# Kernel optimization log

Hardware: AMD Instinct MI355X
Metric: run time of the kernel (lower is better)

## Reference

```python
import jax, jax.numpy as jnp
import numpy as np

N = 4096       # number of nodes (generalizes the hardcoded 116)
E = 131072     # number of edges (avg degree 32)
F_IN = 128     # node_features_num
FS = 64        # feature_size
H = 8          # pair-MLP hidden width


def setup_inputs() -> dict:
    key = jax.random.key(0)
    ks = jax.random.split(key, 6)
    x = jax.random.normal(ks[0], (N, F_IN), dtype=jnp.float32)
    Wlin = jax.random.normal(ks[1], (FS, F_IN), dtype=jnp.float32) * 0.08
    blin = jnp.zeros((FS,), dtype=jnp.float32)
    W1 = jax.random.normal(ks[2], (H, 2 * FS), dtype=jnp.float32) * 0.08
    b1 = jnp.zeros((H,), dtype=jnp.float32)
    W2 = jax.random.normal(ks[3], (1, H), dtype=jnp.float32) * 0.3
    b2 = jnp.zeros((1,), dtype=jnp.float32)
    edge_index = jax.random.randint(ks[4], (2, E), 0, N, dtype=jnp.int32)
    # uniform noise for the concrete/Gumbel-sigmoid sample (torch.rand)
    u = jax.random.uniform(ks[5], (E,), dtype=jnp.float32, minval=1e-6, maxval=1.0 - 1e-6)
    return dict(x=x, Wlin=Wlin, blin=blin, W1=W1, b1=b1, W2=W2, b2=b2,
                edge_index=edge_index, u=u)


def reference(x, Wlin, blin, W1, b1, W2, b2, edge_index, u):
    # node embedding: Linear(F_IN, FS)
    x64 = x @ Wlin.T + blin                                # [N, FS]
    # all-pairs concat + Linear(2*FS, H) rewritten as two small matmuls
    # + broadcasted add (exactly equivalent math, avoids [N*N, 2*FS]).
    h1 = x64 @ W1[:, :FS].T                                # [N, H]
    h2 = x64 @ W1[:, FS:].T                                # [N, H]
    pair = jax.nn.sigmoid(h1[:, None, :] + h2[None, :, :] + b1)  # [N, N, H]
    score = jax.nn.sigmoid(jnp.einsum('ijh,h->ij', pair, W2[0]) + b2[0])  # [N, N]
    sym = 0.5 * (score + score.T)
    w = sym[edge_index[0], edge_index[1]]                  # [E]
    # _sample_graph, training=True, temperature=0.5, bias=0.0 -> bias=1e-4
    bias = 0.0001
    eps = (2.0 * bias - 1.0) * u + (1.0 - bias)            # eps in (1e-4, 1-1e-4)
    gate = jax.nn.sigmoid((jnp.log(eps) - jnp.log1p(-eps) + w) / 0.5)
    pos_penalty = jnp.var(gate, ddof=1)                    # torch.var is unbiased
    return gate, pos_penalty
```

## Files before the change

kernel.cpp:

```cpp
#include <hip/hip_runtime.h>
#include <math.h>

#define NNODES 4096
#define EEDGES 131072
#define FIN    128
#define FS     64

__device__ __forceinline__ float sigmoidf_(float x) {
    return 1.0f / (1.0f + __expf(-x));
}

__global__ void fuse_weights(const float* __restrict__ W1,
                             const float* __restrict__ Wlin,
                             const float* __restrict__ blin,
                             const float* __restrict__ b1,
                             float* __restrict__ M,
                             float* __restrict__ dvec) {
    int idx = blockIdx.x * blockDim.x + threadIdx.x;
    if (idx < 16 * FIN) {
        int k = idx >> 7;
        int c = idx & 127;
        const float* w1row = (k < 8) ? (W1 + k * 128) : (W1 + (k - 8) * 128 + 64);
        float acc = 0.f;
        #pragma unroll 8
        for (int f = 0; f < FS; ++f)
            acc = fmaf(w1row[f], Wlin[f * FIN + c], acc);
        M[idx] = acc;
    } else if (idx < 16 * FIN + 16) {
        int k = idx - 16 * FIN;
        const float* w1row = (k < 8) ? (W1 + k * 128) : (W1 + (k - 8) * 128 + 64);
        float acc = 0.f;
        #pragma unroll 8
        for (int f = 0; f < FS; ++f)
            acc = fmaf(w1row[f], blin[f], acc);
        if (k < 8) acc += b1[k];
        dvec[k] = acc;
    }
}

__global__ void node_mlp(const float* __restrict__ x,
                         const float* __restrict__ M,
                         const float* __restrict__ dvec,
                         float* __restrict__ h) {
    int t = blockIdx.x * blockDim.x + threadIdx.x;
    int n = t >> 4;
    int k = t & 15;
    const float4* xr = (const float4*)(x + n * FIN);
    const float4* mr = (const float4*)(M + k * FIN);
    float acc = dvec[k];
    #pragma unroll
    for (int q = 0; q < FIN / 4; ++q) {
        float4 a = xr[q];
        float4 b = mr[q];
        acc = fmaf(a.x, b.x, acc);
        acc = fmaf(a.y, b.y, acc);
        acc = fmaf(a.z, b.z, acc);
        acc = fmaf(a.w, b.w, acc);
    }
    h[t] = acc;
}

__global__ void edge_kernel(const float* __restrict__ h,
                            const int* __restrict__ ei,
                            const float* __restrict__ u,
                            const float* __restrict__ W2,
                            const float* __restrict__ b2,
                            float* __restrict__ gate,
                            float* __restrict__ partials) {
    int e = blockIdx.x * blockDim.x + threadIdx.x;
    int i = ei[e];
    int j = ei[EEDGES + e];

    const float4* hi = (const float4*)(h + i * 16);
    const float4* hj = (const float4*)(h + j * 16);
    float A1[8], A2[8], B1[8], B2[8];
    *(float4*)(A1)     = hi[0];  *(float4*)(A1 + 4) = hi[1];
    *(float4*)(A2)     = hi[2];  *(float4*)(A2 + 4) = hi[3];
    *(float4*)(B1)     = hj[0];  *(float4*)(B1 + 4) = hj[1];
    *(float4*)(B2)     = hj[2];  *(float4*)(B2 + 4) = hj[3];

    float w2v[8];
    *(float4*)(w2v)     = ((const float4*)W2)[0];
    *(float4*)(w2v + 4) = ((const float4*)W2)[1];
    float b2v = b2[0];

    float tij = 0.f, tji = 0.f;
    #pragma unroll
    for (int k = 0; k < 8; ++k) {
        tij = fmaf(w2v[k], sigmoidf_(A1[k] + B2[k]), tij);
        tji = fmaf(w2v[k], sigmoidf_(B1[k] + A2[k]), tji);
    }
    float sij = sigmoidf_(tij + b2v);
    float sji = sigmoidf_(tji + b2v);
    float w = 0.5f * (sij + sji);

    float uv = u[e];
    float eps = fmaf(-0.9998f, uv, 0.9999f);
    float logit = __logf(eps) - log1pf(-eps);
    float g = sigmoidf_(2.0f * (logit + w));
    gate[e] = g;

    float s = g, s2 = g * g;
    #pragma unroll
    for (int off = 32; off > 0; off >>= 1) {
        s  += __shfl_down(s,  off, 64);
        s2 += __shfl_down(s2, off, 64);
    }
    __shared__ float ls[4], ls2[4];
    int wave = threadIdx.x >> 6;
    if ((threadIdx.x & 63) == 0) { ls[wave] = s; ls2[wave] = s2; }
    __syncthreads();
    if (threadIdx.x == 0) {
        float ts = ls[0] + ls[1] + ls[2] + ls[3];
        float ts2 = ls2[0] + ls2[1] + ls2[2] + ls2[3];
        partials[blockIdx.x] = ts;
        partials[512 + blockIdx.x] = ts2;
    }
}

__global__ void finalize(const float* __restrict__ partials,
                         float* __restrict__ out) {
    int t = threadIdx.x;
    float s  = partials[t]       + partials[t + 256];
    float s2 = partials[512 + t] + partials[512 + t + 256];
    #pragma unroll
    for (int off = 32; off > 0; off >>= 1) {
        s  += __shfl_down(s,  off, 64);
        s2 += __shfl_down(s2, off, 64);
    }
    __shared__ float ls[4], ls2[4];
    int wave = t >> 6;
    if ((t & 63) == 0) { ls[wave] = s; ls2[wave] = s2; }
    __syncthreads();
    if (t == 0) {
        float S  = ls[0] + ls[1] + ls[2] + ls[3];
        float S2 = ls2[0] + ls2[1] + ls2[2] + ls2[3];
        const float Ef = (float)EEDGES;
        float var = (S2 - S * S / Ef) / (Ef - 1.0f);
        out[EEDGES] = var;
    }
}

extern "C" void kernel_launch(void* const* d_in, const int* in_sizes, int n_in,
                              void* d_out, int out_size, void* d_ws, size_t ws_size,
                              hipStream_t stream) {
    const float* x    = (const float*)d_in[0];
    const float* Wlin = (const float*)d_in[1];
    const float* blin = (const float*)d_in[2];
    const float* W1   = (const float*)d_in[3];
    const float* b1   = (const float*)d_in[4];
    const float* W2   = (const float*)d_in[5];
    const float* b2   = (const float*)d_in[6];
    const int*   ei   = (const int*)d_in[7];
    const float* u    = (const float*)d_in[8];
    float* out = (float*)d_out;

    float* ws       = (float*)d_ws;
    float* M        = ws;
    float* dvec     = ws + 2048;
    float* h        = ws + 2064;
    float* partials = ws + 2064 + 65536;

    fuse_weights<<<9, 256, 0, stream>>>(W1, Wlin, blin, b1, M, dvec);
    node_mlp<<<256, 256, 0, stream>>>(x, M, dvec, h);
    edge_kernel<<<512, 256, 0, stream>>>(h, ei, u, W2, b2, out, partials);
    finalize<<<1, 256, 0, stream>>>(partials, out);
}
```

Measured before the change: 87.85 us.

## Fuse weight folding into node kernel and finalize into edge kernel

Each node block now recomputes the folded weight matrix into shared memory instead of using a separate kernel, removing one launch. The variance finalize is folded into the edge kernel through a last-block-done atomic counter, removing another launch. log1pf is replaced by a direct log of a precomputed 1-eps. In exchange every node block does redundant weight folding (about 2K dot products of length 64), and the finalize now depends on correct fence and atomic ordering.

```diff
diff --git a/kernel.cpp b/kernel.cpp
--- a/kernel.cpp
+++ b/kernel.cpp
@@ -5,49 +5,56 @@
 #define EEDGES 131072
 #define FIN    128
 #define FS     64
+#define EBLOCKS 512
 
 __device__ __forceinline__ float sigmoidf_(float x) {
     return 1.0f / (1.0f + __expf(-x));
 }
 
-__global__ void fuse_weights(const float* __restrict__ W1,
-                             const float* __restrict__ Wlin,
-                             const float* __restrict__ blin,
-                             const float* __restrict__ b1,
-                             float* __restrict__ M,
-                             float* __restrict__ dvec) {
-    int idx = blockIdx.x * blockDim.x + threadIdx.x;
-    if (idx < 16 * FIN) {
-        int k = idx >> 7;
-        int c = idx & 127;
+__global__ __launch_bounds__(256) void fused_node(
+        const float* __restrict__ x,
+        const float* __restrict__ Wlin,
+        const float* __restrict__ blin,
+        const float* __restrict__ W1,
+        const float* __restrict__ b1,
+        float* __restrict__ h,
+        unsigned int* __restrict__ counter) {
+    __shared__ float Msh[16 * 132];
+    __shared__ float dsh[16];
+    int tid = threadIdx.x;
+
+    if (blockIdx.x == 0 && tid == 0) {
+        __hip_atomic_store(counter, 0u, __ATOMIC_RELAXED, __HIP_MEMORY_SCOPE_AGENT);
+    }
+
+    #pragma unroll
+    for (int p = 0; p < 8; ++p) {
+        int e = tid + p * 256;
+        int k = e >> 7;
+        int c = e & 127;
         const float* w1row = (k < 8) ? (W1 + k * 128) : (W1 + (k - 8) * 128 + 64);
         float acc = 0.f;
-        #pragma unroll 8
+        #pragma unroll 16
         for (int f = 0; f < FS; ++f)
             acc = fmaf(w1row[f], Wlin[f * FIN + c], acc);
-        M[idx] = acc;
-    } else if (idx < 16 * FIN + 16) {
-        int k = idx - 16 * FIN;
+        Msh[k * 132 + c] = acc;
+    }
+    if (tid < 16) {
+        int k = tid;
         const float* w1row = (k < 8) ? (W1 + k * 128) : (W1 + (k - 8) * 128 + 64);
-        float acc = 0.f;
-        #pragma unroll 8
+        float acc = (k < 8) ? b1[k] : 0.f;
+        #pragma unroll 16
         for (int f = 0; f < FS; ++f)
             acc = fmaf(w1row[f], blin[f], acc);
-        if (k < 8) acc += b1[k];
-        dvec[k] = acc;
+        dsh[k] = acc;
     }
-}
+    __syncthreads();
 
-__global__ void node_mlp(const float* __restrict__ x,
-                         const float* __restrict__ M,
-                         const float* __restrict__ dvec,
-                         float* __restrict__ h) {
-    int t = blockIdx.x * blockDim.x + threadIdx.x;
-    int n = t >> 4;
-    int k = t & 15;
+    int n = (blockIdx.x << 4) + (tid >> 4);
+    int k = tid & 15;
     const float4* xr = (const float4*)(x + n * FIN);
-    const float4* mr = (const float4*)(M + k * FIN);
-    float acc = dvec[k];
+    const float4* mr = (const float4*)(Msh + k * 132);
+    float acc = dsh[k];
     #pragma unroll
     for (int q = 0; q < FIN / 4; ++q) {
         float4 a = xr[q];
@@ -57,22 +64,25 @@
         acc = fmaf(a.z, b.z, acc);
         acc = fmaf(a.w, b.w, acc);
     }
-    h[t] = acc;
+    h[(n << 4) + k] = acc;
 }
 
-__global__ void edge_kernel(const float* __restrict__ h,
-                            const int* __restrict__ ei,
-                            const float* __restrict__ u,
-                            const float* __restrict__ W2,
-                            const float* __restrict__ b2,
-                            float* __restrict__ gate,
-                            float* __restrict__ partials) {
-    int e = blockIdx.x * blockDim.x + threadIdx.x;
+__global__ __launch_bounds__(256) void edge_kernel(
+        const float* __restrict__ h,
+        const int* __restrict__ ei,
+        const float* __restrict__ u,
+        const float* __restrict__ W2,
+        const float* __restrict__ b2,
+        float* __restrict__ out,
+        float* __restrict__ partials,
+        unsigned int* __restrict__ counter) {
+    int tid = threadIdx.x;
+    int e = blockIdx.x * 256 + tid;
     int i = ei[e];
     int j = ei[EEDGES + e];
 
-    const float4* hi = (const float4*)(h + i * 16);
-    const float4* hj = (const float4*)(h + j * 16);
+    const float4* hi = (const float4*)(h + (i << 4));
+    const float4* hj = (const float4*)(h + (j << 4));
     float A1[8], A2[8], B1[8], B2[8];
     *(float4*)(A1)     = hi[0];  *(float4*)(A1 + 4) = hi[1];
     *(float4*)(A2)     = hi[2];  *(float4*)(A2 + 4) = hi[3];
@@ -90,15 +100,14 @@
         tij = fmaf(w2v[k], sigmoidf_(A1[k] + B2[k]), tij);
         tji = fmaf(w2v[k], sigmoidf_(B1[k] + A2[k]), tji);
     }
-    float sij = sigmoidf_(tij + b2v);
-    float sji = sigmoidf_(tji + b2v);
-    float w = 0.5f * (sij + sji);
+    float w = 0.5f * (sigmoidf_(tij + b2v) + sigmoidf_(tji + b2v));
 
     float uv = u[e];
-    float eps = fmaf(-0.9998f, uv, 0.9999f);
-    float logit = __logf(eps) - log1pf(-eps);
+    float eps       = fmaf(-0.9998f, uv, 0.9999f);
+    float one_m_eps = fmaf( 0.9998f, uv, 0.0001f);
+    float logit = __logf(eps) - __logf(one_m_eps);
     float g = sigmoidf_(2.0f * (logit + w));
-    gate[e] = g;
+    out[e] = g;
 
     float s = g, s2 = g * g;
     #pragma unroll
@@ -107,37 +116,41 @@
         s2 += __shfl_down(s2, off, 64);
     }
     __shared__ float ls[4], ls2[4];
-    int wave = threadIdx.x >> 6;
-    if ((threadIdx.x & 63) == 0) { ls[wave] = s; ls2[wave] = s2; }
+    int wave = tid >> 6;
+    if ((tid & 63) == 0) { ls[wave] = s; ls2[wave] = s2; }
     __syncthreads();
-    if (threadIdx.x == 0) {
-        float ts = ls[0] + ls[1] + ls[2] + ls[3];
+
+    __shared__ unsigned int lastFlag;
+    if (tid == 0) {
+        float ts  = ls[0] + ls[1] + ls[2] + ls[3];
         float ts2 = ls2[0] + ls2[1] + ls2[2] + ls2[3];
-        partials[blockIdx.x] = ts;
-        partials[512 + blockIdx.x] = ts2;
+        __hip_atomic_store(&partials[blockIdx.x],       ts,  __ATOMIC_RELAXED, __HIP_MEMORY_SCOPE_AGENT);
+        __hip_atomic_store(&partials[EBLOCKS + blockIdx.x], ts2, __ATOMIC_RELAXED, __HIP_MEMORY_SCOPE_AGENT);
+        __threadfence();
+        unsigned int old = __hip_atomic_fetch_add(counter, 1u, __ATOMIC_ACQ_REL, __HIP_MEMORY_SCOPE_AGENT);
+        lastFlag = (old == (unsigned)(gridDim.x - 1)) ? 1u : 0u;
     }
-}
+    __syncthreads();
 
-__global__ void finalize(const float* __restrict__ partials,
-                         float* __restrict__ out) {
-    int t = threadIdx.x;
-    float s  = partials[t]       + partials[t + 256];
-    float s2 = partials[512 + t] + partials[512 + t + 256];
-    #pragma unroll
-    for (int off = 32; off > 0; off >>= 1) {
-        s  += __shfl_down(s,  off, 64);
-        s2 += __shfl_down(s2, off, 64);
-    }
-    __shared__ float ls[4], ls2[4];
-    int wave = t >> 6;
-    if ((t & 63) == 0) { ls[wave] = s; ls2[wave] = s2; }
-    __syncthreads();
-    if (t == 0) {
-        float S  = ls[0] + ls[1] + ls[2] + ls[3];
-        float S2 = ls2[0] + ls2[1] + ls2[2] + ls2[3];
-        const float Ef = (float)EEDGES;
-        float var = (S2 - S * S / Ef) / (Ef - 1.0f);
-        out[EEDGES] = var;
+    if (lastFlag) {
+        float fs  = __hip_atomic_load(&partials[tid],           __ATOMIC_RELAXED, __HIP_MEMORY_SCOPE_AGENT)
+                  + __hip_atomic_load(&partials[tid + 256],     __ATOMIC_RELAXED, __HIP_MEMORY_SCOPE_AGENT);
+        float fs2 = __hip_atomic_load(&partials[EBLOCKS + tid],       __ATOMIC_RELAXED, __HIP_MEMORY_SCOPE_AGENT)
+                  + __hip_atomic_load(&partials[EBLOCKS + tid + 256], __ATOMIC_RELAXED, __HIP_MEMORY_SCOPE_AGENT);
+        #pragma unroll
+        for (int off = 32; off > 0; off >>= 1) {
+            fs  += __shfl_down(fs,  off, 64);
+            fs2 += __shfl_down(fs2, off, 64);
+        }
+        if ((tid & 63) == 0) { ls[wave] = fs; ls2[wave] = fs2; }
+        __syncthreads();
+        if (tid == 0) {
+            float S  = ls[0] + ls[1] + ls[2] + ls[3];
+            float S2 = ls2[0] + ls2[1] + ls2[2] + ls2[3];
+            const float Ef = (float)EEDGES;
+            float var = (S2 - S * S / Ef) / (Ef - 1.0f);
+            out[EEDGES] = var;
+        }
     }
 }
 
@@ -156,13 +169,10 @@
     float* out = (float*)d_out;
 
     float* ws       = (float*)d_ws;
-    float* M        = ws;
-    float* dvec     = ws + 2048;
-    float* h        = ws + 2064;
-    float* partials = ws + 2064 + 65536;
+    float* h        = ws;
+    float* partials = ws + 65536;
+    unsigned int* counter = (unsigned int*)(ws + 65536 + 1024);
 
-    fuse_weights<<<9, 256, 0, stream>>>(W1, Wlin, blin, b1, M, dvec);
-    node_mlp<<<256, 256, 0, stream>>>(x, M, dvec, h);
-    edge_kernel<<<512, 256, 0, stream>>>(h, ei, u, W2, b2, out, partials);
-    finalize<<<1, 256, 0, stream>>>(partials, out);
+    fused_node<<<NNODES / 16, 256, 0, stream>>>(x, Wlin, blin, W1, b1, h, counter);
+    edge_kernel<<<EBLOCKS, 256, 0, stream>>>(h, ei, u, W2, b2, out, partials, counter);
 }
```

New measurement: 106.8 us. 1.22x slower.
